# Kernel optimization log

Measured on AMD Instinct MI355X. Metric: run time of the kernel, lower is better.

## Reference

```python
import jax, jax.numpy as jnp
import numpy as np

N_NODES = 50000
N_EDGES = 600000
D = 128
NUM_LAYERS = 2
ALPHA = 0.5
EPS = 1e-12  # torch F.normalize eps


def setup_inputs() -> dict:
    key = jax.random.key(0)
    k1, k2, k3, k4, k5 = jax.random.split(key, 5)
    x = jax.random.normal(k1, (N_NODES, D), dtype=jnp.float32)
    edge_attr = jax.random.normal(k2, (N_EDGES, D), dtype=jnp.float32)
    question_emb = jax.random.normal(k3, (D,), dtype=jnp.float32)
    src = jax.random.randint(k4, (N_EDGES,), 0, N_NODES)
    dst = jax.random.randint(k5, (N_EDGES,), 0, N_NODES)
    edge_index = jnp.stack([src, dst], axis=0).astype(jnp.int64)
    return {"x": x, "edge_attr": edge_attr, "question_emb": question_emb, "edge_index": edge_index}


def reference(x, edge_attr, question_emb, edge_index):
    num_nodes = x.shape[0]
    # edge similarity: cosine of edge_attr rows vs question vector
    ea = edge_attr / jnp.maximum(jnp.linalg.norm(edge_attr, axis=1, keepdims=True), EPS)
    q = question_emb / jnp.maximum(jnp.linalg.norm(question_emb), EPS)
    edge_sim = ea @ q  # [E]
    src, dst = edge_index[0], edge_index[1]
    # degree of destination nodes (constant across layers)
    deg = jax.ops.segment_sum(jnp.ones_like(edge_sim), dst, num_segments=num_nodes)
    deg = jnp.clip(deg, 1.0)[:, None]  # [N,1]
    for _ in range(NUM_LAYERS):
        msgs = x[src] * edge_sim[:, None]                              # [E,D] gather + scale
        x_new = jax.ops.segment_sum(msgs, dst, num_segments=num_nodes)  # [N,D] scatter-add
        x_new = x_new / deg                                             # mean aggregation
        x = ALPHA * x + (1.0 - ALPHA) * x_new                           # residual blend
    return x
```

## Files before the change

kernel.cpp:

```cpp
#include <hip/hip_runtime.h>
#include <math.h>

#define N_NODES 50000
#define N_EDGES 600000
#define D 128
#define EPS 1e-12f

#define SCAN_B 256
#define N_SCAN_BLOCKS ((N_NODES + SCAN_B - 1) / SCAN_B)

__global__ void qnorm_kernel(const float* __restrict__ q, float* __restrict__ qn) {
    __shared__ float red[2];
    int t = threadIdx.x;
    float v = q[t];
    float ss = v * v;
    #pragma unroll
    for (int off = 32; off > 0; off >>= 1) ss += __shfl_down(ss, off);
    if ((t & 63) == 0) red[t >> 6] = ss;
    __syncthreads();
    float inv = 1.0f / fmaxf(sqrtf(red[0] + red[1]), EPS);
    qn[t] = v * inv;
}

__global__ void edge_sim_kernel(const float* __restrict__ ea,
                                const float* __restrict__ qn,
                                float* __restrict__ sim) {
    int gid  = blockIdx.x * blockDim.x + threadIdx.x;
    int wave = gid >> 6;
    int lane = threadIdx.x & 63;
    if (wave >= N_EDGES) return;
    const float2 v = ((const float2*)(ea + (size_t)wave * D))[lane];
    const float2 q = ((const float2*)qn)[lane];
    float dot = v.x * q.x + v.y * q.y;
    float ss  = v.x * v.x + v.y * v.y;
    #pragma unroll
    for (int off = 32; off > 0; off >>= 1) {
        dot += __shfl_down(dot, off);
        ss  += __shfl_down(ss, off);
    }
    if (lane == 0) sim[wave] = dot / fmaxf(sqrtf(ss), EPS);
}

__global__ void count_kernel(const int* __restrict__ dst, int* __restrict__ cnt) {
    int e = blockIdx.x * blockDim.x + threadIdx.x;
    if (e < N_EDGES) atomicAdd(&cnt[dst[e]], 1);
}

__global__ void deg_inv_kernel(const int* __restrict__ cnt, float* __restrict__ deg_inv) {
    int n = blockIdx.x * blockDim.x + threadIdx.x;
    if (n < N_NODES) deg_inv[n] = 1.0f / fmaxf((float)cnt[n], 1.0f);
}

__global__ void block_sum_kernel(const int* __restrict__ cnt, int* __restrict__ bsum) {
    __shared__ int s[SCAN_B];
    int t = threadIdx.x;
    int i = blockIdx.x * SCAN_B + t;
    s[t] = (i < N_NODES) ? cnt[i] : 0;
    __syncthreads();
    for (int off = SCAN_B / 2; off > 0; off >>= 1) {
        if (t < off) s[t] += s[t + off];
        __syncthreads();
    }
    if (t == 0) bsum[blockIdx.x] = s[0];
}

__global__ void scan_bsums_kernel(int* __restrict__ bsum) {
    __shared__ int s[SCAN_B];
    int t = threadIdx.x;
    int v = (t < N_SCAN_BLOCKS) ? bsum[t] : 0;
    s[t] = v;
    __syncthreads();
    for (int off = 1; off < SCAN_B; off <<= 1) {
        int a = (t >= off) ? s[t - off] : 0;
        __syncthreads();
        s[t] += a;
        __syncthreads();
    }
    if (t < N_SCAN_BLOCKS) bsum[t] = s[t] - v;
}

__global__ void scan_final_kernel(const int* __restrict__ cnt,
                                  const int* __restrict__ bsum,
                                  int* __restrict__ row_ptr) {
    __shared__ int s[SCAN_B];
    int t = threadIdx.x;
    int i = blockIdx.x * SCAN_B + t;
    int v = (i < N_NODES) ? cnt[i] : 0;
    s[t] = v;
    __syncthreads();
    for (int off = 1; off < SCAN_B; off <<= 1) {
        int a = (t >= off) ? s[t - off] : 0;
        __syncthreads();
        s[t] += a;
        __syncthreads();
    }
    if (i < N_NODES) row_ptr[i] = s[t] - v + bsum[blockIdx.x];
    if (i == N_NODES - 1) row_ptr[N_NODES] = N_EDGES;
}

__global__ void fill_kernel(const int* __restrict__ src, const int* __restrict__ dst,
                            const float* __restrict__ sim,
                            int* __restrict__ cursor,
                            int* __restrict__ csr_src, float* __restrict__ csr_sim) {
    int e = blockIdx.x * blockDim.x + threadIdx.x;
    if (e >= N_EDGES) return;
    int d = dst[e];
    int idx = atomicAdd(&cursor[d], 1);
    csr_src[idx] = src[e];
    csr_sim[idx] = sim[e];
}

__global__ void agg_kernel(const float* __restrict__ xin,
                           const int* __restrict__ row_ptr,
                           const int* __restrict__ csr_src,
                           const float* __restrict__ csr_sim,
                           const float* __restrict__ deg_inv,
                           float* __restrict__ xout) {
    int gid  = blockIdx.x * blockDim.x + threadIdx.x;
    int node = gid >> 6;
    int lane = threadIdx.x & 63;
    if (node >= N_NODES) return;
    int beg = row_ptr[node];
    int end = row_ptr[node + 1];
    float2 acc = make_float2(0.0f, 0.0f);
    int j = beg;
    for (; j + 1 < end; j += 2) {
        int   s0 = csr_src[j],     s1 = csr_src[j + 1];
        float w0 = csr_sim[j],     w1 = csr_sim[j + 1];
        float2 v0 = ((const float2*)(xin + (size_t)s0 * D))[lane];
        float2 v1 = ((const float2*)(xin + (size_t)s1 * D))[lane];
        acc.x += v0.x * w0 + v1.x * w1;
        acc.y += v0.y * w0 + v1.y * w1;
    }
    if (j < end) {
        int   s0 = csr_src[j];
        float w0 = csr_sim[j];
        float2 v0 = ((const float2*)(xin + (size_t)s0 * D))[lane];
        acc.x += v0.x * w0;
        acc.y += v0.y * w0;
    }
    float di = deg_inv[node];
    float2 a = ((const float2*)(xin + (size_t)node * D))[lane];
    float2 o;
    o.x = 0.5f * a.x + 0.5f * acc.x * di;
    o.y = 0.5f * a.y + 0.5f * acc.y * di;
    ((float2*)(xout + (size_t)node * D))[lane] = o;
}

extern "C" void kernel_launch(void* const* d_in, const int* in_sizes, int n_in,
                              void* d_out, int out_size, void* d_ws, size_t ws_size,
                              hipStream_t stream) {
    const float* x  = (const float*)d_in[0];
    const float* ea = (const float*)d_in[1];
    const float* q  = (const float*)d_in[2];
    const int*   ei = (const int*)d_in[3];
    const int* src = ei;
    const int* dst = ei + N_EDGES;
    float* out = (float*)d_out;

    float* x1       = (float*)d_ws;
    float* sim      = x1 + (size_t)N_NODES * D;
    float* csr_sim  = sim + N_EDGES;
    float* deg_inv  = csr_sim + N_EDGES;
    float* qn       = deg_inv + N_NODES;
    int*   cnt      = (int*)(qn + 128);
    int*   row_ptr  = cnt + N_NODES;
    int*   cursor   = row_ptr + N_NODES + 1;
    int*   bsum     = cursor + N_NODES;
    int*   csr_src  = bsum + 256;

    hipMemsetAsync(cnt, 0, (size_t)N_NODES * sizeof(int), stream);

    qnorm_kernel<<<1, 128, 0, stream>>>(q, qn);

    {
        long long threads = (long long)N_EDGES * 64;
        int blocks = (int)((threads + 255) / 256);
        edge_sim_kernel<<<blocks, 256, 0, stream>>>(ea, qn, sim);
    }

    const int eb = (N_EDGES + 255) / 256;
    count_kernel<<<eb, 256, 0, stream>>>(dst, cnt);
    deg_inv_kernel<<<(N_NODES + 255) / 256, 256, 0, stream>>>(cnt, deg_inv);

    block_sum_kernel<<<N_SCAN_BLOCKS, SCAN_B, 0, stream>>>(cnt, bsum);
    scan_bsums_kernel<<<1, SCAN_B, 0, stream>>>(bsum);
    scan_final_kernel<<<N_SCAN_BLOCKS, SCAN_B, 0, stream>>>(cnt, bsum, row_ptr);

    hipMemcpyAsync(cursor, row_ptr, (size_t)N_NODES * sizeof(int),
                   hipMemcpyDeviceToDevice, stream);
    fill_kernel<<<eb, 256, 0, stream>>>(src, dst, sim, cursor, csr_src, csr_sim);

    const int agg_blocks = (int)(((long long)N_NODES * 64 + 255) / 256);
    agg_kernel<<<agg_blocks, 256, 0, stream>>>(x,  row_ptr, csr_src, csr_sim, deg_inv, x1);
    agg_kernel<<<agg_blocks, 256, 0, stream>>>(x1, row_ptr, csr_src, csr_sim, deg_inv, out);
}
```

Measured before the change: 635.6 us.

## Fuse degree counting into edge-sim, widen loads, and preload CSR indices in aggregation

The edge similarity kernel now processes two edges per wavefront with float4 loads and also performs the destination degree atomic count, which removes the separate count kernel. The scan kernel writes the cursor and inverse degree directly, eliminating the deg_inv kernel and the device-to-device memcpy. The aggregation kernel splits each wave into two halves that each handle alternate neighbours with float4 loads, preloads up to 64 neighbour indices and weights once and broadcasts them with shuffles, then combines the halves with a cross-half shuffle. This cuts launch count and per-edge index-load latency, at the cost of idle half-wave lanes during the final write and extra shuffle work.

Result: faster. 563.9 us (-11.3%).

```diff
diff --git a/kernel.cpp b/kernel.cpp
--- a/kernel.cpp
+++ b/kernel.cpp
@@ -24,31 +24,30 @@
 
 __global__ void edge_sim_kernel(const float* __restrict__ ea,
                                 const float* __restrict__ qn,
-                                float* __restrict__ sim) {
+                                const int* __restrict__ dst,
+                                float* __restrict__ sim,
+                                int* __restrict__ cnt) {
     int gid  = blockIdx.x * blockDim.x + threadIdx.x;
     int wave = gid >> 6;
+    if (wave >= N_EDGES / 2) return;
     int lane = threadIdx.x & 63;
-    if (wave >= N_EDGES) return;
-    const float2 v = ((const float2*)(ea + (size_t)wave * D))[lane];
-    const float2 q = ((const float2*)qn)[lane];
-    float dot = v.x * q.x + v.y * q.y;
-    float ss  = v.x * v.x + v.y * v.y;
+    int half = lane >> 5;
+    int l32  = lane & 31;
+    int e    = 2 * wave + half;
+
+    float4 v = ((const float4*)(ea + (size_t)e * D))[l32];
+    float4 q = ((const float4*)qn)[l32];
+    float dot = v.x * q.x + v.y * q.y + v.z * q.z + v.w * q.w;
+    float ss  = v.x * v.x + v.y * v.y + v.z * v.z + v.w * v.w;
     #pragma unroll
-    for (int off = 32; off > 0; off >>= 1) {
-        dot += __shfl_down(dot, off);
-        ss  += __shfl_down(ss, off);
-    }
-    if (lane == 0) sim[wave] = dot / fmaxf(sqrtf(ss), EPS);
-}
-
-__global__ void count_kernel(const int* __restrict__ dst, int* __restrict__ cnt) {
-    int e = blockIdx.x * blockDim.x + threadIdx.x;
-    if (e < N_EDGES) atomicAdd(&cnt[dst[e]], 1);
-}
-
-__global__ void deg_inv_kernel(const int* __restrict__ cnt, float* __restrict__ deg_inv) {
-    int n = blockIdx.x * blockDim.x + threadIdx.x;
-    if (n < N_NODES) deg_inv[n] = 1.0f / fmaxf((float)cnt[n], 1.0f);
+    for (int off = 16; off > 0; off >>= 1) {
+        dot += __shfl_xor(dot, off);
+        ss  += __shfl_xor(ss, off);
+    }
+    if (l32 == 0) {
+        sim[e] = dot / fmaxf(sqrtf(ss), EPS);
+        atomicAdd(&cnt[dst[e]], 1);
+    }
 }
 
 __global__ void block_sum_kernel(const int* __restrict__ cnt, int* __restrict__ bsum) {
@@ -81,7 +80,9 @@
 
 __global__ void scan_final_kernel(const int* __restrict__ cnt,
                                   const int* __restrict__ bsum,
-                                  int* __restrict__ row_ptr) {
+                                  int* __restrict__ row_ptr,
+                                  int* __restrict__ cursor,
+                                  float* __restrict__ deg_inv) {
     __shared__ int s[SCAN_B];
     int t = threadIdx.x;
     int i = blockIdx.x * SCAN_B + t;
@@ -94,7 +95,12 @@
         s[t] += a;
         __syncthreads();
     }
-    if (i < N_NODES) row_ptr[i] = s[t] - v + bsum[blockIdx.x];
+    if (i < N_NODES) {
+        int rp = s[t] - v + bsum[blockIdx.x];
+        row_ptr[i] = rp;
+        cursor[i]  = rp;
+        deg_inv[i] = 1.0f / fmaxf((float)v, 1.0f);
+    }
     if (i == N_NODES - 1) row_ptr[N_NODES] = N_EDGES;
 }
 
@@ -118,33 +124,48 @@
                            float* __restrict__ xout) {
     int gid  = blockIdx.x * blockDim.x + threadIdx.x;
     int node = gid >> 6;
+    if (node >= N_NODES) return;
     int lane = threadIdx.x & 63;
-    if (node >= N_NODES) return;
+    int half = lane >> 5;
+    int l32  = lane & 31;
+
     int beg = row_ptr[node];
     int end = row_ptr[node + 1];
-    float2 acc = make_float2(0.0f, 0.0f);
-    int j = beg;
-    for (; j + 1 < end; j += 2) {
-        int   s0 = csr_src[j],     s1 = csr_src[j + 1];
-        float w0 = csr_sim[j],     w1 = csr_sim[j + 1];
-        float2 v0 = ((const float2*)(xin + (size_t)s0 * D))[lane];
-        float2 v1 = ((const float2*)(xin + (size_t)s1 * D))[lane];
-        acc.x += v0.x * w0 + v1.x * w1;
-        acc.y += v0.y * w0 + v1.y * w1;
-    }
-    if (j < end) {
-        int   s0 = csr_src[j];
-        float w0 = csr_sim[j];
-        float2 v0 = ((const float2*)(xin + (size_t)s0 * D))[lane];
-        acc.x += v0.x * w0;
-        acc.y += v0.y * w0;
-    }
-    float di = deg_inv[node];
-    float2 a = ((const float2*)(xin + (size_t)node * D))[lane];
-    float2 o;
-    o.x = 0.5f * a.x + 0.5f * acc.x * di;
-    o.y = 0.5f * a.y + 0.5f * acc.y * di;
-    ((float2*)(xout + (size_t)node * D))[lane] = o;
+    int n   = end - beg;
+
+    int   sl = 0; float wl = 0.0f;
+    if (lane < n) { sl = csr_src[beg + lane]; wl = csr_sim[beg + lane]; }
+
+    float4 acc = make_float4(0.0f, 0.0f, 0.0f, 0.0f);
+    int nn = (n < 64) ? n : 64;
+    #pragma unroll 2
+    for (int j = half; j < nn; j += 2) {
+        int   s = __shfl(sl, j);
+        float w = __shfl(wl, j);
+        float4 v = ((const float4*)(xin + (size_t)s * D))[l32];
+        acc.x += v.x * w; acc.y += v.y * w; acc.z += v.z * w; acc.w += v.w * w;
+    }
+    for (int j = 64 + half; j < n; j += 2) {
+        int   s = csr_src[beg + j];
+        float w = csr_sim[beg + j];
+        float4 v = ((const float4*)(xin + (size_t)s * D))[l32];
+        acc.x += v.x * w; acc.y += v.y * w; acc.z += v.z * w; acc.w += v.w * w;
+    }
+    acc.x += __shfl_xor(acc.x, 32);
+    acc.y += __shfl_xor(acc.y, 32);
+    acc.z += __shfl_xor(acc.z, 32);
+    acc.w += __shfl_xor(acc.w, 32);
+
+    if (half == 0) {
+        float di = deg_inv[node];
+        float4 a = ((const float4*)(xin + (size_t)node * D))[l32];
+        float4 o;
+        o.x = 0.5f * a.x + 0.5f * acc.x * di;
+        o.y = 0.5f * a.y + 0.5f * acc.y * di;
+        o.z = 0.5f * a.z + 0.5f * acc.z * di;
+        o.w = 0.5f * a.w + 0.5f * acc.w * di;
+        ((float4*)(xout + (size_t)node * D))[l32] = o;
+    }
 }
 
 extern "C" void kernel_launch(void* const* d_in, const int* in_sizes, int n_in,
@@ -174,22 +195,16 @@
     qnorm_kernel<<<1, 128, 0, stream>>>(q, qn);
 
     {
-        long long threads = (long long)N_EDGES * 64;
+        long long threads = (long long)(N_EDGES / 2) * 64;
         int blocks = (int)((threads + 255) / 256);
-        edge_sim_kernel<<<blocks, 256, 0, stream>>>(ea, qn, sim);
-    }
-
-    const int eb = (N_EDGES + 255) / 256;
-    count_kernel<<<eb, 256, 0, stream>>>(dst, cnt);
-    deg_inv_kernel<<<(N_NODES + 255) / 256, 256, 0, stream>>>(cnt, deg_inv);
+        edge_sim_kernel<<<blocks, 256, 0, stream>>>(ea, qn, dst, sim, cnt);
+    }
 
     block_sum_kernel<<<N_SCAN_BLOCKS, SCAN_B, 0, stream>>>(cnt, bsum);
     scan_bsums_kernel<<<1, SCAN_B, 0, stream>>>(bsum);
-    scan_final_kernel<<<N_SCAN_BLOCKS, SCAN_B, 0, stream>>>(cnt, bsum, row_ptr);
-
-    hipMemcpyAsync(cursor, row_ptr, (size_t)N_NODES * sizeof(int),
-                   hipMemcpyDeviceToDevice, stream);
-    fill_kernel<<<eb, 256, 0, stream>>>(src, dst, sim, cursor, csr_src, csr_sim);
+    scan_final_kernel<<<N_SCAN_BLOCKS, SCAN_B, 0, stream>>>(cnt, bsum, row_ptr, cursor, deg_inv);
+
+    fill_kernel<<<(N_EDGES + 255) / 256, 256, 0, stream>>>(src, dst, sim, cursor, csr_src, csr_sim);
 
     const int agg_blocks = (int)(((long long)N_NODES * 64 + 255) / 256);
     agg_kernel<<<agg_blocks, 256, 0, stream>>>(x,  row_ptr, csr_src, csr_sim, deg_inv, x1);
```
